# Kernel optimization log

Measured on AMD Instinct MI355X. Metric: run time of the kernel, lower is better.

## Reference

```python
import jax, jax.numpy as jnp
import numpy as np

B, D, H, C, P, HP = 65536, 256, 512, 10, 10, 128


def setup_inputs() -> dict:
    key = jax.random.key(0)
    ks = jax.random.split(key, 6)
    return {
        "x": jax.random.normal(ks[0], (B, D), jnp.float32),
        "Wt1": jax.random.normal(ks[1], (D, H), jnp.float32) * (1.0 / np.sqrt(D)),
        "bt1": jnp.zeros((H,), jnp.float32),
        "Wt2": jax.random.normal(ks[2], (H, C), jnp.float32) * (1.0 / np.sqrt(H)),
        "bt2": jnp.zeros((C,), jnp.float32),
        "Wp1": jax.random.normal(ks[3], (P, D, HP), jnp.float32) * (1.0 / np.sqrt(D)),
        "bp1": jnp.zeros((P, HP), jnp.float32),
        "Wp2": jax.random.normal(ks[4], (P, HP, C), jnp.float32) * (1.0 / np.sqrt(HP)),
        "bp2": jnp.zeros((P, C), jnp.float32),
        "repair_direction_dict": jax.random.randint(ks[5], (P, 2), 0, C, jnp.int32),
    }


def _get_bitmap(out, rdd):
    # torch.topk(out, 2): indices of the two largest logits per row
    _, idx = jax.lax.top_k(out, 2)                                  # [B, 2]
    # is_in[b, p] = all(idx[b] == rdd[p])  (exact top-2 pair match)
    is_in = jnp.all(idx[:, None, :] == rdd[None, :, :], axis=-1)     # [B, P]
    no_match = ~jnp.any(is_in, axis=-1)                              # [B]
    # fallback for unmatched rows: top-1 index equals rdd[:, 0]
    fallback = idx[:, :1] == rdd[None, :, 0]                         # [B, P]
    return jnp.where(no_match[:, None], fallback, is_in)             # bool [B, P]


def reference(x, Wt1, bt1, Wt2, bt2, Wp1, bp1, Wp2, bp2, repair_direction_dict):
    # target net forward: out = target_net(x)
    out = jnp.maximum(x @ Wt1 + bt1, 0.0) @ Wt2 + bt2                # [B, C]
    # bitmap computed under no_grad in the original -> stop_gradient
    bitmap = jax.lax.stop_gradient(
        _get_bitmap(out, repair_direction_dict)
    ).astype(out.dtype)                                              # [B, P]
    # each patch net runs on the FULL batch (as in the original), then the
    # bitmap gates the scatter-add combine: out[bits] += p_out[bits]
    h = jnp.maximum(jnp.einsum('bd,pdh->pbh', x, Wp1) + bp1[:, None, :], 0.0)  # [P, B, HP]
    p_out = jnp.einsum('pbh,phc->pbc', h, Wp2) + bp2[:, None, :]     # [P, B, C]
    return out + jnp.einsum('bp,pbc->bc', bitmap, p_out)             # [B, C]
```

## Files before the change

### kernel.cpp

```cpp
#include <hip/hip_runtime.h>

typedef unsigned int u32;
typedef unsigned short u16;
typedef _Float16 f16;
typedef __attribute__((ext_vector_type(8))) _Float16 f16x8;
typedef __attribute__((ext_vector_type(4))) float f32x4;

#define MARGIN 1e-2f
#define LSC 2048.0f
#define LSCI (1.0f/2048.0f)

__device__ __forceinline__ u16 f16b(float f) {
    return __builtin_bit_cast(u16, (f16)f);
}
__device__ __forceinline__ f32x4 MF(f16x8 a, f16x8 b, f32x4 c) {
    return __builtin_amdgcn_mfma_f32_16x16x32_f16(a, b, c, 0, 0, 0);
}
__device__ __forceinline__ uint4 pack8(const u16 v[8]) {
    uint4 pk;
    pk.x = (u32)v[0] | ((u32)v[1] << 16);
    pk.y = (u32)v[2] | ((u32)v[3] << 16);
    pk.z = (u32)v[4] | ((u32)v[5] << 16);
    pk.w = (u32)v[6] | ((u32)v[7] << 16);
    return pk;
}
__device__ __forceinline__ f16x8 l2afrag(const u16* s, int kf, int quad, int row) {
    union { u16 q[8]; f16x8 v; } u;
    #pragma unroll
    for (int j = 0; j < 8; ++j) u.q[j] = s[(kf * 32 + quad * 8 + j) * 72 + row];
    return u.v;
}

__global__ __launch_bounds__(256) void conv_kernel(
    const float* __restrict__ Wt1, const float* __restrict__ Wp1,
    const float* __restrict__ Wt2, const float* __restrict__ Wp2,
    u16* __restrict__ wt1f, u16* __restrict__ wt1g, u16* __restrict__ wp1f,
    u16* __restrict__ wt2f, u16* __restrict__ wt2g, u16* __restrict__ wp2f,
    u32* __restrict__ gcnt)
{
    __shared__ float tile[64][68];
    const int t = threadIdx.x;
    const int b = blockIdx.x;

    if (b == 112) {
        if (t == 0) gcnt[0] = 0;
        for (int cc = t; cc < 1024; cc += 256) {
            int kk = cc >> 6, l = cc & 63, ln = l & 15, quad = l >> 4;
            u16 vh[8], vl[8];
            #pragma unroll
            for (int j = 0; j < 8; ++j) {
                int k = kk * 32 + quad * 8 + j;
                float f = (ln < 10) ? Wt2[k * 10 + ln] : 0.f;
                f16 h = (f16)f;
                vh[j] = __builtin_bit_cast(u16, h);
                vl[j] = f16b(LSC * (f - (float)h));
            }
            *(uint4*)(wt2f + kk * 512 + l * 8) = pack8(vh);
            *(uint4*)(wt2g + kk * 512 + l * 8) = pack8(vl);
        }
        for (int cc = t; cc < 2560; cc += 256) {
            int p = cc >> 8, rem = cc & 255, kk = rem >> 6, l = rem & 63;
            int ln = l & 15, quad = (l >> 4) & 3;
            u16 v[8];
            #pragma unroll
            for (int j = 0; j < 8; ++j) {
                int k = kk * 32 + quad * 8 + j;
                v[j] = f16b(ln < 10 ? Wp2[p * 1280 + k * 10 + ln] : 0.f);
            }
            *(uint4*)(wp2f + p * 2048 + kk * 512 + l * 8) = pack8(v);
        }
        return;
    }

    const float* src; int src_ld;
    u16 *dsth, *dstl; int nf0, kk0;
    if (b < 32) {
        int kt = b & 3, nt = b >> 2;
        src = Wt1 + (size_t)(kt * 64) * 512 + nt * 64; src_ld = 512;
        dsth = wt1f; dstl = wt1g; nf0 = nt * 4; kk0 = kt * 2;
    } else {
        int j = b - 32, p = j >> 3, r = j & 7;
        int kt = r & 3, nt = r >> 2;
        src = Wp1 + (size_t)p * 32768 + (size_t)(kt * 64) * 128 + nt * 64; src_ld = 128;
        dsth = wp1f + p * 32768; dstl = nullptr; nf0 = nt * 4; kk0 = kt * 2;
    }
    {
        const int kr = t >> 2, c0 = (t & 3) * 16;
        #pragma unroll
        for (int u = 0; u < 4; ++u) {
            float4 v = *(const float4*)(src + (size_t)kr * src_ld + c0 + u * 4);
            tile[kr][c0 + u*4 + 0] = v.x;
            tile[kr][c0 + u*4 + 1] = v.y;
            tile[kr][c0 + u*4 + 2] = v.z;
            tile[kr][c0 + u*4 + 3] = v.w;
        }
    }
    __syncthreads();
    #pragma unroll
    for (int s = 0; s < 2; ++s) {
        int cc = t + 256 * s;
        int l = cc & 63, fp = cc >> 6, nfl = fp >> 1, kkl = fp & 1;
        int ln = l & 15, quad = (l >> 4) & 3;
        int nloc = nfl * 16 + ln, kloc = kkl * 32 + quad * 8;
        u16 vh[8], vl[8];
        #pragma unroll
        for (int j = 0; j < 8; ++j) {
            float f = tile[kloc + j][nloc];
            f16 h = (f16)f;
            vh[j] = __builtin_bit_cast(u16, h);
            vl[j] = f16b(LSC * (f - (float)h));
        }
        size_t off = (size_t)((nf0 + nfl) * 8 + (kk0 + kkl)) * 512 + l * 8;
        *(uint4*)(dsth + off) = pack8(vh);
        if (dstl) *(uint4*)(dstl + off) = pack8(vl);
    }
}

#define LDQ(Q,J) (*(const f16x8*)(wt1f + (size_t)((Q)*64 + h2*32 + (J)) * 512 + lane*8))
#define LDT(Q,K2) (*(const f16x8*)(wt2f + (size_t)((Q)*4+(K2))*512 + lane*8))

#define HSTORE(Q,NFL) { \
    const int colL = (h2*4+(NFL))*16 + ln; \
    const float bias = bt1[(Q)*128 + colL]; \
    ushort4 hv_; \
    { float h_=acc[0]+bias; h_=h_>0.f?h_:0.f; hv_.x=f16b(h_); } \
    { float h_=acc[1]+bias; h_=h_>0.f?h_:0.f; hv_.y=f16b(h_); } \
    { float h_=acc[2]+bias; h_=h_>0.f?h_:0.f; hv_.z=f16b(h_); } \
    { float h_=acc[3]+bias; h_=h_>0.f?h_:0.f; hv_.w=f16b(h_); } \
    *(ushort4*)(scratch + colL*72 + mg*16 + quad*4) = hv_; }

#define NFB_STD(Q,NFL) { f32x4 acc={0.f,0.f,0.f,0.f}; \
    acc=MF(a0,bA,acc); bA=LDQ(Q,(NFL)*8+4); \
    acc=MF(a1,bB,acc); bB=LDQ(Q,(NFL)*8+5); \
    acc=MF(a2,bC,acc); bC=LDQ(Q,(NFL)*8+6); \
    acc=MF(a3,bD,acc); bD=LDQ(Q,(NFL)*8+7); \
    acc=MF(a4,bA,acc); bA=LDQ(Q,(NFL)*8+8); \
    acc=MF(a5,bB,acc); bB=LDQ(Q,(NFL)*8+9); \
    acc=MF(a6,bC,acc); bC=LDQ(Q,(NFL)*8+10); \
    acc=MF(a7,bD,acc); bD=LDQ(Q,(NFL)*8+11); \
    HSTORE(Q,NFL) }

#define NFB_LAST(Q,QN) { f32x4 acc={0.f,0.f,0.f,0.f}; \
    acc=MF(a0,bA,acc); bA=LDQ(Q,28); \
    acc=MF(a1,bB,acc); bB=LDQ(Q,29); \
    acc=MF(a2,bC,acc); bC=LDQ(Q,30); \
    acc=MF(a3,bD,acc); bD=LDQ(Q,31); \
    acc=MF(a4,bA,acc); bA=LDQ(QN,0); \
    acc=MF(a5,bB,acc); bB=LDQ(QN,1); \
    acc=MF(a6,bC,acc); bC=LDQ(QN,2); \
    acc=MF(a7,bD,acc); bD=LDQ(QN,3); \
    HSTORE(Q,3) }

#define QUARTER9(Q,QN,LASTQ) \
    NFB_STD(Q,0) NFB_STD(Q,1) NFB_STD(Q,2) NFB_LAST(Q,QN) \
    __syncthreads(); \
    if (w < 4) { \
        f16x8 A0_=l2afrag(scratch,0,quad,w*16+ln), A1_=l2afrag(scratch,1,quad,w*16+ln); \
        f16x8 A2_=l2afrag(scratch,2,quad,w*16+ln), A3_=l2afrag(scratch,3,quad,w*16+ln); \
        acc2=MF(A0_,t0,acc2); acc2=MF(A1_,t1,acc2); \
        acc2=MF(A2_,t2,acc2); acc2=MF(A3_,t3,acc2); \
        if (!(LASTQ)) { t0=LDT((Q)+1,0); t1=LDT((Q)+1,1); t2=LDT((Q)+1,2); t3=LDT((Q)+1,3); } \
    } \
    __syncthreads();

__global__ __launch_bounds__(512, 2) void netsum_kernel(
    const float* __restrict__ x, const float* __restrict__ bt1,
    const float* __restrict__ bt2,
    const float* __restrict__ bp1, const float* __restrict__ bp2,
    const int* __restrict__ rdd,
    const u16* __restrict__ wt1f, const u16* __restrict__ wp1f,
    const u16* __restrict__ wt2f, const u16* __restrict__ wp2f,
    float* __restrict__ out, u32* __restrict__ gcnt, u32* __restrict__ glist)
{
    __shared__ u16 xf[64][264];
    __shared__ u16 scratch[17920];
    __shared__ float lg[64][10];
    __shared__ float oacc[64][10];
    __shared__ u32 plist[10][64];
    __shared__ u32 pcnt[10];
    __shared__ int rdds[20];
    __shared__ u32 wq[40];
    __shared__ u32 nwork;

    const int t = threadIdx.x;
    const int lane = t & 63;
    const int w = t >> 6;
    const int ln = lane & 15;
    const int quad = lane >> 4;
    const int mg = w & 3;
    const int h2 = w >> 2;
    const int row0 = blockIdx.x * 64;

    if (t < 10) pcnt[t] = 0;
    if (t < 20) rdds[t] = rdd[t];
    if (t == 0) nwork = 0;
    for (int i = t; i < 640; i += 512) ((float*)oacc)[i] = 0.f;

    #pragma unroll
    for (int i = 0; i < 8; ++i) {
        int f = t + 512 * i;
        int r = f >> 6, c4 = f & 63;
        float4 v = *(const float4*)(x + (size_t)(row0 + r) * 256 + c4 * 4);
        u16 q0 = f16b(v.x), q1 = f16b(v.y), q2 = f16b(v.z), q3 = f16b(v.w);
        uint2 pw = { (u32)q0 | ((u32)q1 << 16), (u32)q2 | ((u32)q3 << 16) };
        *(uint2*)&xf[r][c4 * 4] = pw;
    }
    f16x8 bA = LDQ(0,0), bB = LDQ(0,1), bC = LDQ(0,2), bD = LDQ(0,3);
    f16x8 t0 = {}, t1 = {}, t2 = {}, t3 = {};
    if (w < 4) { t0 = LDT(0,0); t1 = LDT(0,1); t2 = LDT(0,2); t3 = LDT(0,3); }
    __syncthreads();

    f16x8 a0 = *(const f16x8*)(&xf[mg*16+ln][0*32 + quad*8]);
    f16x8 a1 = *(const f16x8*)(&xf[mg*16+ln][1*32 + quad*8]);
    f16x8 a2 = *(const f16x8*)(&xf[mg*16+ln][2*32 + quad*8]);
    f16x8 a3 = *(const f16x8*)(&xf[mg*16+ln][3*32 + quad*8]);
    f16x8 a4 = *(const f16x8*)(&xf[mg*16+ln][4*32 + quad*8]);
    f16x8 a5 = *(const f16x8*)(&xf[mg*16+ln][5*32 + quad*8]);
    f16x8 a6 = *(const f16x8*)(&xf[mg*16+ln][6*32 + quad*8]);
    f16x8 a7 = *(const f16x8*)(&xf[mg*16+ln][7*32 + quad*8]);

    f32x4 acc2 = (f32x4){0.f, 0.f, 0.f, 0.f};
    QUARTER9(0,1,0)
    QUARTER9(1,2,0)
    QUARTER9(2,3,0)
    QUARTER9(3,3,1)
    if (w < 4 && ln < 10) {
        #pragma unroll
        for (int r = 0; r < 4; ++r)
            lg[w * 16 + quad * 4 + r][ln] = acc2[r] + bt2[ln];
    }
    __syncthreads();

    if (t < 64) {
        float l[10];
        #pragma unroll
        for (int c = 0; c < 10; ++c) l[c] = lg[t][c];
        float b0v = -1e30f; int i0 = 0;
        #pragma unroll
        for (int c = 0; c < 10; ++c) if (l[c] > b0v) { b0v = l[c]; i0 = c; }
        float b1v = -1e30f; int i1 = 0;
        #pragma unroll
        for (int c = 0; c < 10; ++c) { if (c == i0) continue; if (l[c] > b1v) { b1v = l[c]; i1 = c; } }
        float b2v = -1e30f;
        #pragma unroll
        for (int c = 0; c < 10; ++c) { if (c == i0 || c == i1) continue; if (l[c] > b2v) b2v = l[c]; }
        if (b0v - b1v < MARGIN || b1v - b2v < MARGIN) {
            u32 idx = atomicAdd(gcnt, 1u);
            glist[idx] = (u32)(row0 + t);
        }
        u32 exact = 0, fb = 0;
        #pragma unroll
        for (int p = 0; p < 10; ++p) {
            int a = rdds[2 * p], bq = rdds[2 * p + 1];
            if (i0 == a && i1 == bq) exact |= 1u << p;
            if (i0 == a)             fb    |= 1u << p;
        }
        u32 bits = exact ? exact : fb;
        while (bits) {
            int p = __ffs(bits) - 1;
            bits &= bits - 1;
            u32 idx = atomicAdd(&pcnt[p], 1u);
            plist[p][idx] = (u32)t;
        }
    }
    __syncthreads();
    if (t < 10) {
        int L = (int)pcnt[t];
        for (int base = 0; base < L; base += 16) {
            u32 e = atomicAdd(&nwork, 1u);
            wq[e] = ((u32)t << 8) | (u32)base;
        }
    }
    __syncthreads();

    {
        const u32 nw = nwork;
        for (u32 ii = w; ii < nw; ii += 8) {
            const u32 item = wq[ii];
            const int p = (int)(item >> 8), mbase = (int)(item & 255);
            const int Lp = (int)pcnt[p];
            const int mi = mbase + ln;
            const int arow = (mi < Lp) ? (int)plist[p][mi] : (int)plist[p][0];
            const u16* xr = &xf[arow][0];
            const u16* wb = wp1f + (size_t)p * 32768 + (size_t)lane * 8;
            u16* hp = &scratch[w * 2176];
            #pragma unroll
            for (int g = 0; g < 2; ++g) {
                f32x4 acc4[4];
                #pragma unroll
                for (int i2 = 0; i2 < 4; ++i2) acc4[i2] = (f32x4){0.f,0.f,0.f,0.f};
                f16x8 wc4[4];
                #pragma unroll
                for (int i2 = 0; i2 < 4; ++i2)
                    wc4[i2] = *(const f16x8*)(wb + ((g * 4 + i2) * 8 + 0) * 512);
                #pragma unroll
                for (int kk = 0; kk < 8; ++kk) {
                    f16x8 wn4[4];
                    #pragma unroll
                    for (int i2 = 0; i2 < 4; ++i2) {
                        wn4[i2] = wc4[i2];
                        if (kk < 7)
                            wn4[i2] = *(const f16x8*)(wb + ((g * 4 + i2) * 8 + kk + 1) * 512);
                    }
                    f16x8 a = *(const f16x8*)(xr + kk * 32 + quad * 8);
                    #pragma unroll
                    for (int i2 = 0; i2 < 4; ++i2) acc4[i2] = MF(a, wc4[i2], acc4[i2]);
                    #pragma unroll
                    for (int i2 = 0; i2 < 4; ++i2) wc4[i2] = wn4[i2];
                }
                #pragma unroll
                for (int i2 = 0; i2 < 4; ++i2) {
                    const int i2g = g * 4 + i2;
                    float bias = bp1[p * 128 + i2g * 16 + ln];
                    #pragma unroll
                    for (int r = 0; r < 4; ++r) {
                        float hv = acc4[i2][r] + bias; hv = hv > 0.f ? hv : 0.f;
                        hp[(quad * 4 + r) * 136 + i2g * 16 + ln] = f16b(hv);
                    }
                }
            }
            f32x4 po = (f32x4){0.f,0.f,0.f,0.f};
            #pragma unroll
            for (int kk = 0; kk < 4; ++kk) {
                f16x8 ha = *(const f16x8*)(&hp[ln * 136 + kk * 32 + quad * 8]);
                f16x8 wb2 = *(const f16x8*)(wp2f + p * 2048 + kk * 512 + lane * 8);
                po = MF(ha, wb2, po);
            }
            if (ln < 10) {
                float b2 = bp2[p * 10 + ln];
                #pragma unroll
                for (int r = 0; r < 4; ++r) {
                    int mi2 = mbase + quad * 4 + r;
                    if (mi2 < Lp)
                        atomicAdd(&oacc[plist[p][mi2]][ln], po[r] + b2);
                }
            }
        }
    }
    __syncthreads();

    for (int i = t; i < 640; i += 512)
        out[(size_t)row0 * 10 + i] = ((float*)lg)[i] + ((float*)oacc)[i];
}

#define FLD(S,KK) \
    S##h0 = *(const f16x8*)(bbh + (KK)*512); \
    S##h1 = *(const f16x8*)(bbh + 4096 + (KK)*512); \
    S##l0 = *(const f16x8*)(bbl + (KK)*512); \
    S##l1 = *(const f16x8*)(bbl + 4096 + (KK)*512);
#define FCP(S,KK) { _Pragma("unroll") for (int m_=0;m_<4;++m_){ \
    f16x8 ah_=*(const f16x8*)(&xfh[m_*16+ln][(KK)*32+quad*8]); \
    f16x8 al_=*(const f16x8*)(&xfl[m_*16+ln][(KK)*32+quad*8]); \
    accH[m_][0]=MF(ah_,S##h0,accH[m_][0]); accS[m_][0]=MF(ah_,S##l0,accS[m_][0]); accS[m_][0]=MF(al_,S##h0,accS[m_][0]); \
    accH[m_][1]=MF(ah_,S##h1,accH[m_][1]); accS[m_][1]=MF(ah_,S##l1,accS[m_][1]); accS[m_][1]=MF(al_,S##h1,accS[m_][1]); } }
#define F2L(WH, WL, KK) \
    WH = *(const f16x8*)(wt2f + (hl*8+(KK))*512 + lane*8); \
    WL = *(const f16x8*)(wt2g + (hl*8+(KK))*512 + lane*8);
#define F2C(WH, WL, KK) { int hidx_=(w*16+ln)*264 + (KK)*32 + quad*8; \
    f16x8 hah_=*(const f16x8*)(&hb2[0][hidx_]); f16x8 hal_=*(const f16x8*)(&hb2[1][hidx_]); \
    acc2h=MF(hah_,WH,acc2h); acc2s=MF(hah_,WL,acc2s); acc2s=MF(hal_,WH,acc2s); }

__global__ __launch_bounds__(512, 1) void fix_kernel(
    const float* __restrict__ x, const float* __restrict__ bt1,
    const float* __restrict__ bt2,
    const float* __restrict__ bp1, const float* __restrict__ bp2,
    const int* __restrict__ rdd,
    const u16* __restrict__ wt1f, const u16* __restrict__ wt1g,
    const u16* __restrict__ wt2f, const u16* __restrict__ wt2g,
    const u16* __restrict__ wp1f, const u16* __restrict__ wp2f,
    const u32* __restrict__ gcnt, const u32* __restrict__ glist,
    float* __restrict__ out)
{
    __shared__ u16 xfh[64][264];
    __shared__ u16 xfl[64][264];
    __shared__ u16 hb2[2][16896];
    __shared__ float lg[64][10];
    __shared__ float oacc[64][10];
    __shared__ u32 rows[64];
    __shared__ u32 plist[10][64];
    __shared__ u32 pcnt[10];
    __shared__ int rdds[20];
    __shared__ u32 wq[40];
    __shared__ u32 nwork;

    const int t = threadIdx.x;
    const int lane = t & 63;
    const int w = t >> 6;
    const int ln = lane & 15;
    const int quad = lane >> 4;
    const u32 cnt = gcnt[0];
    if (t < 20) rdds[t] = rdd[t];

    for (u32 base = blockIdx.x * 64; base < cnt; base += gridDim.x * 64) {
        __syncthreads();
        const int R = (int)min(64u, cnt - base);
        if (t < 64) rows[t] = glist[base + (t < R ? t : 0)];
        if (t < 10) pcnt[t] = 0;
        if (t == 0) nwork = 0;
        for (int i = t; i < 640; i += 512) ((float*)oacc)[i] = 0.f;
        __syncthreads();

        #pragma unroll
        for (int i = 0; i < 8; ++i) {
            int f = t + 512 * i;
            int r = f >> 6, c4 = f & 63;
            float4 v = *(const float4*)(x + (size_t)rows[r] * 256 + c4 * 4);
            f16 h0 = (f16)v.x, h1 = (f16)v.y, h2 = (f16)v.z, h3 = (f16)v.w;
            u16 q0 = __builtin_bit_cast(u16, h0), q1 = __builtin_bit_cast(u16, h1);
            u16 q2 = __builtin_bit_cast(u16, h2), q3 = __builtin_bit_cast(u16, h3);
            u16 l0 = f16b(LSC * (v.x - (float)h0)), l1 = f16b(LSC * (v.y - (float)h1));
            u16 l2 = f16b(LSC * (v.z - (float)h2)), l3 = f16b(LSC * (v.w - (float)h3));
            uint2 hw = { (u32)q0 | ((u32)q1 << 16), (u32)q2 | ((u32)q3 << 16) };
            uint2 lw = { (u32)l0 | ((u32)l1 << 16), (u32)l2 | ((u32)l3 << 16) };
            *(uint2*)&xfh[r][c4 * 4] = hw;
            *(uint2*)&xfl[r][c4 * 4] = lw;
        }
        __syncthreads();

        f32x4 acc2h = (f32x4){0.f,0.f,0.f,0.f};
        f32x4 acc2s = (f32x4){0.f,0.f,0.f,0.f};
        for (int hl = 0; hl < 2; ++hl) {
            f32x4 accH[4][2], accS[4][2];
            #pragma unroll
            for (int m = 0; m < 4; ++m)
                #pragma unroll
                for (int i2 = 0; i2 < 2; ++i2) {
                    accH[m][i2] = (f32x4){0.f,0.f,0.f,0.f};
                    accS[m][i2] = (f32x4){0.f,0.f,0.f,0.f};
                }
            const size_t boff = (size_t)(hl * 16 + w * 2) * 4096 + (size_t)lane * 8;
            const u16* bbh = wt1f + boff;
            const u16* bbl = wt1g + boff;
            f16x8 ch0, ch1, cl0, cl1, nh0, nh1, nl0, nl1;
            FLD(c,0);
            FLD(n,1); FCP(c,0);
            FLD(c,2); FCP(n,1);
            FLD(n,3); FCP(c,2);
            FLD(c,4); FCP(n,3);
            FLD(n,5); FCP(c,4);
            FLD(c,6); FCP(n,5);
            FLD(n,7); FCP(c,6);
            FCP(n,7);
            #pragma unroll
            for (int m = 0; m < 4; ++m)
                #pragma unroll
                for (int i2 = 0; i2 < 2; ++i2) {
                    int nloc = w * 32 + i2 * 16 + ln;
                    float bias = bt1[hl * 256 + nloc];
                    #pragma unroll
                    for (int r = 0; r < 4; ++r) {
                        float hv = accH[m][i2][r] + accS[m][i2][r] * LSCI + bias;
                        hv = hv > 0.f ? hv : 0.f;
                        f16 hh = (f16)hv;
                        int idx = (m * 16 + quad * 4 + r) * 264 + nloc;
                        hb2[0][idx] = __builtin_bit_cast(u16, hh);
                        hb2[1][idx] = f16b(LSC * (hv - (float)hh));
                    }
                }
            __syncthreads();
            if (w < 4) {
                f16x8 whc, wlc, whn, wln;
                F2L(whc, wlc, 0);
                F2L(whn, wln, 1); F2C(whc, wlc, 0);
                F2L(whc, wlc, 2); F2C(whn, wln, 1);
                F2L(whn, wln, 3); F2C(whc, wlc, 2);
                F2L(whc, wlc, 4); F2C(whn, wln, 3);
                F2L(whn, wln, 5); F2C(whc, wlc, 4);
                F2L(whc, wlc, 6); F2C(whn, wln, 5);
                F2L(whn, wln, 7); F2C(whc, wlc, 6);
                F2C(whn, wln, 7);
            }
            __syncthreads();
        }
        if (w < 4 && ln < 10) {
            #pragma unroll
            for (int r = 0; r < 4; ++r)
                lg[w * 16 + quad * 4 + r][ln] = acc2h[r] + acc2s[r] * LSCI + bt2[ln];
        }
        __syncthreads();

        if (t < R) {
            float l[10];
            #pragma unroll
            for (int c = 0; c < 10; ++c) l[c] = lg[t][c];
            float b0v = -1e30f; int i0 = 0;
            #pragma unroll
            for (int c = 0; c < 10; ++c) if (l[c] > b0v) { b0v = l[c]; i0 = c; }
            float b1v = -1e30f; int i1 = 0;
            #pragma unroll
            for (int c = 0; c < 10; ++c) { if (c == i0) continue; if (l[c] > b1v) { b1v = l[c]; i1 = c; } }
            u32 exact = 0, fb = 0;
            #pragma unroll
            for (int p = 0; p < 10; ++p) {
                int a = rdds[2 * p], bq = rdds[2 * p + 1];
                if (i0 == a && i1 == bq) exact |= 1u << p;
                if (i0 == a)             fb    |= 1u << p;
            }
            u32 bits = exact ? exact : fb;
            while (bits) {
                int p = __ffs(bits) - 1;
                bits &= bits - 1;
                u32 idx = atomicAdd(&pcnt[p], 1u);
                plist[p][idx] = (u32)t;
            }
        }
        __syncthreads();
        if (t < 10) {
            int L = (int)pcnt[t];
            for (int b2i = 0; b2i < L; b2i += 16) {
                u32 e = atomicAdd(&nwork, 1u);
                wq[e] = ((u32)t << 8) | (u32)b2i;
            }
        }
        __syncthreads();

        {
            const u32 nw = nwork;
            u16* hbase = &hb2[0][0];
            for (u32 ii = w; ii < nw; ii += 8) {
                const u32 item = wq[ii];
                const int p = (int)(item >> 8), mbase = (int)(item & 255);
                const int Lp = (int)pcnt[p];
                const int mi = mbase + ln;
                const int arow = (mi < Lp) ? (int)plist[p][mi] : (int)plist[p][0];
                const u16* xr = &xfh[arow][0];
                const u16* wb = wp1f + (size_t)p * 32768 + (size_t)lane * 8;
                u16* hp = hbase + w * 2176;
                #pragma unroll
                for (int g = 0; g < 2; ++g) {
                    f32x4 acc4[4];
                    #pragma unroll
                    for (int i2 = 0; i2 < 4; ++i2) acc4[i2] = (f32x4){0.f,0.f,0.f,0.f};
                    f16x8 wc4[4];
                    #pragma unroll
                    for (int i2 = 0; i2 < 4; ++i2)
                        wc4[i2] = *(const f16x8*)(wb + ((g * 4 + i2) * 8 + 0) * 512);
                    #pragma unroll
                    for (int kk = 0; kk < 8; ++kk) {
                        f16x8 wn4[4];
                        #pragma unroll
                        for (int i2 = 0; i2 < 4; ++i2) {
                            wn4[i2] = wc4[i2];
                            if (kk < 7)
                                wn4[i2] = *(const f16x8*)(wb + ((g * 4 + i2) * 8 + kk + 1) * 512);
                        }
                        f16x8 a = *(const f16x8*)(xr + kk * 32 + quad * 8);
                        #pragma unroll
                        for (int i2 = 0; i2 < 4; ++i2) acc4[i2] = MF(a, wc4[i2], acc4[i2]);
                        #pragma unroll
                        for (int i2 = 0; i2 < 4; ++i2) wc4[i2] = wn4[i2];
                    }
                    #pragma unroll
                    for (int i2 = 0; i2 < 4; ++i2) {
                        const int i2g = g * 4 + i2;
                        float bias = bp1[p * 128 + i2g * 16 + ln];
                        #pragma unroll
                        for (int r = 0; r < 4; ++r) {
                            float hv = acc4[i2][r] + bias; hv = hv > 0.f ? hv : 0.f;
                            hp[(quad * 4 + r) * 136 + i2g * 16 + ln] = f16b(hv);
                        }
                    }
                }
                f32x4 po = (f32x4){0.f,0.f,0.f,0.f};
                #pragma unroll
                for (int kk = 0; kk < 4; ++kk) {
                    f16x8 ha = *(const f16x8*)(&hp[ln * 136 + kk * 32 + quad * 8]);
                    f16x8 wb2 = *(const f16x8*)(wp2f + p * 2048 + kk * 512 + lane * 8);
                    po = MF(ha, wb2, po);
                }
                if (ln < 10) {
                    float b2 = bp2[p * 10 + ln];
                    #pragma unroll
                    for (int r = 0; r < 4; ++r) {
                        int mi2 = mbase + quad * 4 + r;
                        if (mi2 < Lp)
                            atomicAdd(&oacc[plist[p][mi2]][ln], po[r] + b2);
                    }
                }
            }
        }
        __syncthreads();

        for (int i = t; i < R * 10; i += 512) {
            int r = i / 10, c = i % 10;
            out[(size_t)rows[r] * 10 + c] = lg[r][c] + oacc[r][c];
        }
    }
}

extern "C" void kernel_launch(void* const* d_in, const int* in_sizes, int n_in,
                              void* d_out, int out_size, void* d_ws, size_t ws_size,
                              hipStream_t stream) {
    const float* x   = (const float*)d_in[0];
    const float* Wt1 = (const float*)d_in[1];
    const float* bt1 = (const float*)d_in[2];
    const float* Wt2 = (const float*)d_in[3];
    const float* bt2 = (const float*)d_in[4];
    const float* Wp1 = (const float*)d_in[5];
    const float* bp1 = (const float*)d_in[6];
    const float* Wp2 = (const float*)d_in[7];
    const float* bp2 = (const float*)d_in[8];
    const int* rdd = (const int*)d_in[9];
    float* out = (float*)d_out;

    u16* wt1f = (u16*)d_ws;
    u16* wt1g = wt1f + 131072;
    u16* wp1f = wt1g + 131072;
    u16* wt2f = wp1f + 327680;
    u16* wt2g = wt2f + 8192;
    u16* wp2f = wt2g + 8192;
    u32* gcnt  = (u32*)(wp2f + 20480);
    u32* glist = gcnt + 16;

    hipLaunchKernelGGL(conv_kernel, dim3(113), dim3(256), 0, stream,
                       Wt1, Wp1, Wt2, Wp2, wt1f, wt1g, wp1f, wt2f, wt2g, wp2f, gcnt);
    hipLaunchKernelGGL(netsum_kernel, dim3(1024), dim3(512), 0, stream,
                       x, bt1, bt2, bp1, bp2, rdd,
                       wt1f, wp1f, wt2f, wp2f, out, gcnt, glist);
    hipLaunchKernelGGL(fix_kernel, dim3(256), dim3(512), 0, stream,
                       x, bt1, bt2, bp1, bp2, rdd,
                       wt1f, wt1g, wt2f, wt2g, wp1f, wp2f,
                       gcnt, glist, out);
}
```

Measured before the change: 209.3 us.

## Restructure target-net layer-1 so each wave computes all rows for a column slab

```diff
diff --git a/kernel.cpp b/kernel.cpp
--- a/kernel.cpp
+++ b/kernel.cpp
@@ -24,12 +24,6 @@
     pk.w = (u32)v[6] | ((u32)v[7] << 16);
     return pk;
 }
-__device__ __forceinline__ f16x8 l2afrag(const u16* s, int kf, int quad, int row) {
-    union { u16 q[8]; f16x8 v; } u;
-    #pragma unroll
-    for (int j = 0; j < 8; ++j) u.q[j] = s[(kf * 32 + quad * 8 + j) * 72 + row];
-    return u.v;
-}
 
 __global__ __launch_bounds__(256) void conv_kernel(
     const float* __restrict__ Wt1, const float* __restrict__ Wp1,
@@ -116,54 +110,13 @@
     }
 }
 
-#define LDQ(Q,J) (*(const f16x8*)(wt1f + (size_t)((Q)*64 + h2*32 + (J)) * 512 + lane*8))
 #define LDT(Q,K2) (*(const f16x8*)(wt2f + (size_t)((Q)*4+(K2))*512 + lane*8))
-
-#define HSTORE(Q,NFL) { \
-    const int colL = (h2*4+(NFL))*16 + ln; \
-    const float bias = bt1[(Q)*128 + colL]; \
-    ushort4 hv_; \
-    { float h_=acc[0]+bias; h_=h_>0.f?h_:0.f; hv_.x=f16b(h_); } \
-    { float h_=acc[1]+bias; h_=h_>0.f?h_:0.f; hv_.y=f16b(h_); } \
-    { float h_=acc[2]+bias; h_=h_>0.f?h_:0.f; hv_.z=f16b(h_); } \
-    { float h_=acc[3]+bias; h_=h_>0.f?h_:0.f; hv_.w=f16b(h_); } \
-    *(ushort4*)(scratch + colL*72 + mg*16 + quad*4) = hv_; }
-
-#define NFB_STD(Q,NFL) { f32x4 acc={0.f,0.f,0.f,0.f}; \
-    acc=MF(a0,bA,acc); bA=LDQ(Q,(NFL)*8+4); \
-    acc=MF(a1,bB,acc); bB=LDQ(Q,(NFL)*8+5); \
-    acc=MF(a2,bC,acc); bC=LDQ(Q,(NFL)*8+6); \
-    acc=MF(a3,bD,acc); bD=LDQ(Q,(NFL)*8+7); \
-    acc=MF(a4,bA,acc); bA=LDQ(Q,(NFL)*8+8); \
-    acc=MF(a5,bB,acc); bB=LDQ(Q,(NFL)*8+9); \
-    acc=MF(a6,bC,acc); bC=LDQ(Q,(NFL)*8+10); \
-    acc=MF(a7,bD,acc); bD=LDQ(Q,(NFL)*8+11); \
-    HSTORE(Q,NFL) }
-
-#define NFB_LAST(Q,QN) { f32x4 acc={0.f,0.f,0.f,0.f}; \
-    acc=MF(a0,bA,acc); bA=LDQ(Q,28); \
-    acc=MF(a1,bB,acc); bB=LDQ(Q,29); \
-    acc=MF(a2,bC,acc); bC=LDQ(Q,30); \
-    acc=MF(a3,bD,acc); bD=LDQ(Q,31); \
-    acc=MF(a4,bA,acc); bA=LDQ(QN,0); \
-    acc=MF(a5,bB,acc); bB=LDQ(QN,1); \
-    acc=MF(a6,bC,acc); bC=LDQ(QN,2); \
-    acc=MF(a7,bD,acc); bD=LDQ(QN,3); \
-    HSTORE(Q,3) }
-
-#define QUARTER9(Q,QN,LASTQ) \
-    NFB_STD(Q,0) NFB_STD(Q,1) NFB_STD(Q,2) NFB_LAST(Q,QN) \
-    __syncthreads(); \
-    if (w < 4) { \
-        f16x8 A0_=l2afrag(scratch,0,quad,w*16+ln), A1_=l2afrag(scratch,1,quad,w*16+ln); \
-        f16x8 A2_=l2afrag(scratch,2,quad,w*16+ln), A3_=l2afrag(scratch,3,quad,w*16+ln); \
-        acc2=MF(A0_,t0,acc2); acc2=MF(A1_,t1,acc2); \
-        acc2=MF(A2_,t2,acc2); acc2=MF(A3_,t3,acc2); \
-        if (!(LASTQ)) { t0=LDT((Q)+1,0); t1=LDT((Q)+1,1); t2=LDT((Q)+1,2); t3=LDT((Q)+1,3); } \
-    } \
-    __syncthreads();
-
-__global__ __launch_bounds__(512, 2) void netsum_kernel(
+#define L1G(BR, NF, KK) \
+    acc[0][NF]=MF(a0,BR,acc[0][NF]); acc[1][NF]=MF(a1,BR,acc[1][NF]); \
+    acc[2][NF]=MF(a2,BR,acc[2][NF]); acc[3][NF]=MF(a3,BR,acc[3][NF]); \
+    if ((KK)<7) BR = *(const f16x8*)(wb1 + ((NF)*8+(KK)+1)*512);
+
+__global__ __launch_bounds__(512, 4) void netsum_kernel(
     const float* __restrict__ x, const float* __restrict__ bt1,
     const float* __restrict__ bt2,
     const float* __restrict__ bp1, const float* __restrict__ bp2,
@@ -187,8 +140,6 @@
     const int w = t >> 6;
     const int ln = lane & 15;
     const int quad = lane >> 4;
-    const int mg = w & 3;
-    const int h2 = w >> 2;
     const int row0 = blockIdx.x * 64;
 
     if (t < 10) pcnt[t] = 0;
@@ -205,25 +156,60 @@
         uint2 pw = { (u32)q0 | ((u32)q1 << 16), (u32)q2 | ((u32)q3 << 16) };
         *(uint2*)&xf[r][c4 * 4] = pw;
     }
-    f16x8 bA = LDQ(0,0), bB = LDQ(0,1), bC = LDQ(0,2), bD = LDQ(0,3);
+    const u16* wb1 = wt1f + (size_t)(w * 32) * 512 + (size_t)lane * 8;
+    f16x8 bA = *(const f16x8*)(wb1 + 0 * 512);
+    f16x8 bB = *(const f16x8*)(wb1 + 8 * 512);
+    f16x8 bC = *(const f16x8*)(wb1 + 16 * 512);
+    f16x8 bD = *(const f16x8*)(wb1 + 24 * 512);
     f16x8 t0 = {}, t1 = {}, t2 = {}, t3 = {};
     if (w < 4) { t0 = LDT(0,0); t1 = LDT(0,1); t2 = LDT(0,2); t3 = LDT(0,3); }
     __syncthreads();
 
-    f16x8 a0 = *(const f16x8*)(&xf[mg*16+ln][0*32 + quad*8]);
-    f16x8 a1 = *(const f16x8*)(&xf[mg*16+ln][1*32 + quad*8]);
-    f16x8 a2 = *(const f16x8*)(&xf[mg*16+ln][2*32 + quad*8]);
-    f16x8 a3 = *(const f16x8*)(&xf[mg*16+ln][3*32 + quad*8]);
-    f16x8 a4 = *(const f16x8*)(&xf[mg*16+ln][4*32 + quad*8]);
-    f16x8 a5 = *(const f16x8*)(&xf[mg*16+ln][5*32 + quad*8]);
-    f16x8 a6 = *(const f16x8*)(&xf[mg*16+ln][6*32 + quad*8]);
-    f16x8 a7 = *(const f16x8*)(&xf[mg*16+ln][7*32 + quad*8]);
+    f32x4 acc[4][4];
+    #pragma unroll
+    for (int m = 0; m < 4; ++m)
+        #pragma unroll
+        for (int i2 = 0; i2 < 4; ++i2) acc[m][i2] = (f32x4){0.f,0.f,0.f,0.f};
+    #pragma unroll
+    for (int kk = 0; kk < 8; ++kk) {
+        f16x8 a0 = *(const f16x8*)(&xf[ 0 + ln][kk*32 + quad*8]);
+        f16x8 a1 = *(const f16x8*)(&xf[16 + ln][kk*32 + quad*8]);
+        f16x8 a2 = *(const f16x8*)(&xf[32 + ln][kk*32 + quad*8]);
+        f16x8 a3 = *(const f16x8*)(&xf[48 + ln][kk*32 + quad*8]);
+        L1G(bA, 0, kk)
+        L1G(bB, 1, kk)
+        L1G(bC, 2, kk)
+        L1G(bD, 3, kk)
+    }
 
     f32x4 acc2 = (f32x4){0.f, 0.f, 0.f, 0.f};
-    QUARTER9(0,1,0)
-    QUARTER9(1,2,0)
-    QUARTER9(2,3,0)
-    QUARTER9(3,3,1)
+    u16* hq = scratch;
+    for (int q = 0; q < 4; ++q) {
+        if ((w >> 1) == q) {
+            const int nfl0 = (w & 1) * 4;
+            #pragma unroll
+            for (int i2 = 0; i2 < 4; ++i2) {
+                const int colL = (nfl0 + i2) * 16 + ln;
+                const float bias = bt1[q * 128 + colL];
+                #pragma unroll
+                for (int m = 0; m < 4; ++m)
+                    #pragma unroll
+                    for (int r = 0; r < 4; ++r) {
+                        float hv = acc[m][i2][r] + bias; hv = hv > 0.f ? hv : 0.f;
+                        hq[(m * 16 + quad * 4 + r) * 140 + colL] = f16b(hv);
+                    }
+            }
+        }
+        __syncthreads();
+        if (w < 4) {
+            acc2 = MF(*(const f16x8*)(&hq[(w*16+ln)*140 + 0*32 + quad*8]), t0, acc2);
+            acc2 = MF(*(const f16x8*)(&hq[(w*16+ln)*140 + 1*32 + quad*8]), t1, acc2);
+            acc2 = MF(*(const f16x8*)(&hq[(w*16+ln)*140 + 2*32 + quad*8]), t2, acc2);
+            acc2 = MF(*(const f16x8*)(&hq[(w*16+ln)*140 + 3*32 + quad*8]), t3, acc2);
+            if (q < 3) { t0 = LDT(q+1,0); t1 = LDT(q+1,1); t2 = LDT(q+1,2); t3 = LDT(q+1,3); }
+        }
+        __syncthreads();
+    }
     if (w < 4 && ln < 10) {
         #pragma unroll
         for (int r = 0; r < 4; ++r)
@@ -283,7 +269,7 @@
             const int arow = (mi < Lp) ? (int)plist[p][mi] : (int)plist[p][0];
             const u16* xr = &xf[arow][0];
             const u16* wb = wp1f + (size_t)p * 32768 + (size_t)lane * 8;
-            u16* hp = &scratch[w * 2176];
+            u16* hp = &scratch[w * 2240];
             #pragma unroll
             for (int g = 0; g < 2; ++g) {
                 f32x4 acc4[4];
@@ -315,14 +301,14 @@
                     #pragma unroll
                     for (int r = 0; r < 4; ++r) {
                         float hv = acc4[i2][r] + bias; hv = hv > 0.f ? hv : 0.f;
-                        hp[(quad * 4 + r) * 136 + i2g * 16 + ln] = f16b(hv);
+                        hp[(quad * 4 + r) * 140 + i2g * 16 + ln] = f16b(hv);
                     }
                 }
             }
             f32x4 po = (f32x4){0.f,0.f,0.f,0.f};
             #pragma unroll
             for (int kk = 0; kk < 4; ++kk) {
-                f16x8 ha = *(const f16x8*)(&hp[ln * 136 + kk * 32 + quad * 8]);
+                f16x8 ha = *(const f16x8*)(&hp[ln * 140 + kk * 32 + quad * 8]);
                 f16x8 wb2 = *(const f16x8*)(wp2f + p * 2048 + kk * 512 + lane * 8);
                 po = MF(ha, wb2, po);
             }
```

Result: slower. 214.6 us (+2.6%).
